# Kernel tuning notes

Measured on AMD Instinct MI355X. Metric: run time of the kernel, lower is better.

Reference implementation:

```python
import jax, jax.numpy as jnp
import numpy as np
import math

LEVELS = 10
T = 4096              # 2**log2_hashmap_size, log2=12
F = 2                 # n_features_per_level
NMIN, NMAX = 16, 320
HIDDEN = 512
OMEGA = 30.0
COOR_DIM = LEVELS * F + 2   # 22: hash feats + raw coords
_b = math.exp((math.log(NMAX) - math.log(NMIN)) / (LEVELS - 1))
RES = [int(math.floor(NMIN * _b ** l)) for l in range(LEVELS)]
PRIME_Y = np.uint32(2654435761)
MASK = np.uint32(T - 1)


def _hash2(xi, yi):
    # instant-NGP style spatial hash for 2D, uint32 wraparound arithmetic
    return (xi ^ (yi * PRIME_Y)) & MASK


def hash_encode(coords, table):
    # coords: [N,2] in [0,1); table: [LEVELS, T, F]
    feats = []
    for l in range(LEVELS):
        x = coords * RES[l]               # [N,2] continuous grid coords
        x0 = jnp.floor(x)
        w = x - x0                        # bilinear weights in [0,1)
        xi = x0.astype(jnp.uint32)
        x0i, y0i = xi[:, 0], xi[:, 1]
        x1i, y1i = x0i + np.uint32(1), y0i + np.uint32(1)
        tab = table[l]
        f00 = tab[_hash2(x0i, y0i)]       # [N,F] gathers
        f10 = tab[_hash2(x1i, y0i)]
        f01 = tab[_hash2(x0i, y1i)]
        f11 = tab[_hash2(x1i, y1i)]
        wx = w[:, 0:1]
        wy = w[:, 1:2]
        fx0 = f00 + (f10 - f00) * wx
        fx1 = f01 + (f11 - f01) * wx
        feats.append(fx0 + (fx1 - fx0) * wy)
    return jnp.concatenate(feats + [coords], axis=-1)  # [N, COOR_DIM]


def sine(x, w, b):
    # SineLayer.forward: sin(linear(x)); omega_0 is baked into first-layer init
    return jnp.sin(x @ w.T + b)


def _sine_init(key, out_f, in_f, is_first):
    kw, kb = jax.random.split(key)
    if is_first:
        lim = OMEGA / in_f
    else:
        lim = math.sqrt(6.0 / in_f) / OMEGA
    w = jax.random.uniform(kw, (out_f, in_f), jnp.float32, -lim, lim)
    blim = 1.0 / math.sqrt(in_f)
    b = jax.random.uniform(kb, (out_f,), jnp.float32, -blim, blim)
    return w, b


def setup_inputs() -> dict:
    key = jax.random.key(0)
    ks = jax.random.split(key, 8)
    N = 262144
    coords = jax.random.uniform(ks[0], (N, 2), jnp.float32)
    table = jax.random.uniform(ks[1], (LEVELS, T, F), jnp.float32, -1e-4, 1e-4)
    w1, b1 = _sine_init(ks[2], HIDDEN, COOR_DIM, True)
    w2, b2 = _sine_init(ks[3], HIDDEN, HIDDEN, False)
    ws1, bs1 = _sine_init(ks[4], HIDDEN, COOR_DIM + HIDDEN, False)
    ws2, bs2 = _sine_init(ks[5], HIDDEN, HIDDEN, False)
    wo, bo = _sine_init(ks[6], 2, HIDDEN, False)
    return {"coords": coords, "table": table,
            "w1": w1, "b1": b1, "w2": w2, "b2": b2,
            "ws1": ws1, "bs1": bs1, "ws2": ws2, "bs2": bs2,
            "wo": wo, "bo": bo}


def reference(coords, table, w1, b1, w2, b2, ws1, bs1, ws2, bs2, wo, bo):
    h0 = hash_encode(coords, table)            # [N,22]
    h1 = sine(sine(h0, w1, b1), w2, b2)        # first block (n_flayer=2)
    h2 = jnp.concatenate([h1, h0], axis=-1)    # skip connection [N,534]
    h2 = sine(sine(h2, ws1, bs1), ws2, bs2)    # second block (n_slayer=2)
    return sine(h2, wo, bo)                    # [N,2]
```

## Files before the change

kernel.cpp:

```cpp
#include <hip/hip_runtime.h>
#include <hip/hip_bf16.h>
#include <math.h>

#define MBLK    64
#define CHUNK   4096
#define H0_OFF  65536
#define LDSB    (H0_OFF + CHUNK)
#define INV2PI  0.15915494309189535f

#define OFF_W1  0
#define OFF_W2  16384
#define OFF_WS1 (16384+262144)
#define OFF_WS2 (278528+278528)
#define OFF_WO  (557056+262144)
#define NPACK   (819200+8192)

typedef __attribute__((ext_vector_type(8))) short bf16x8;
typedef __attribute__((ext_vector_type(4))) float f32x4;

struct ResArr { int r[10]; };

__device__ __forceinline__ unsigned short f2bf(float f) {
    unsigned u = __float_as_uint(f);
    u += 0x7FFFu + ((u >> 16) & 1u);
    return (unsigned short)(u >> 16);
}
__device__ __forceinline__ float bf2f(unsigned short h) {
    return __uint_as_float(((unsigned)h) << 16);
}
__device__ __forceinline__ float hwsin(float x) {
    float r;
    asm("v_sin_f32 %0, %1" : "=v"(r) : "v"(x));
    return r;
}
__device__ __forceinline__ unsigned pack_bf16_rne(float a, float b) {
    unsigned ua = __float_as_uint(a);
    unsigned ub = __float_as_uint(b);
    ua += 0x7FFFu + ((ua >> 16) & 1u);
    ub += 0x7FFFu + ((ub >> 16) & 1u);
    return __builtin_amdgcn_perm(ub, ua, 0x07060302u);
}

__global__ void pack_weights(const float* __restrict__ w1, const float* __restrict__ w2,
                             const float* __restrict__ ws1, const float* __restrict__ ws2,
                             const float* __restrict__ wo, unsigned short* __restrict__ out)
{
    int i = blockIdx.x * 256 + threadIdx.x;
    if (i >= NPACK) return;
    float v;
    if (i < OFF_WO) {
        int il, KC, K_src, K_valid;
        const float* src;
        if (i < OFF_W2)       { il = i;           KC = 1;  K_src = 22;  K_valid = 22;  src = w1;  }
        else if (i < OFF_WS1) { il = i - OFF_W2;  KC = 16; K_src = 512; K_valid = 512; src = w2;  }
        else if (i < OFF_WS2) { il = i - OFF_WS1; KC = 17; K_src = 534; K_valid = 534; src = ws1; }
        else                  { il = i - OFF_WS2; KC = 16; K_src = 512; K_valid = 512; src = ws2; }
        int blk  = il >> 9, idx = il & 511;
        int lane = idx >> 3, j = idx & 7;
        int nf   = blk & 3;
        int rest = blk >> 2;
        int c    = rest % KC;
        int nb   = rest / KC;
        int n = nb * 64 + nf * 16 + (lane & 15);
        int k = c * 32 + (lane >> 4) * 8 + j;
        v = (k < K_valid) ? src[n * K_src + k] : 0.f;
    } else {
        int j = i - OFF_WO;
        int h = j >> 12, ks = (j >> 9) & 7, lane = (j >> 3) & 63, jj = j & 7;
        int n = lane & 15;
        int k = h * 256 + ks * 32 + (lane >> 4) * 8 + jj;
        v = (n < 2) ? wo[n * 512 + k] : 0.f;
    }
    out[i] = f2bf(v * INV2PI);
}

template<int KSTEPS, bool TAIL, bool PREBAR>
__device__ __forceinline__ void mlp_layer(char* sm, const unsigned short* __restrict__ Wl,
                                          const float* __restrict__ bias,
                                          int wid, int lane)
{
    constexpr int NC = KSTEPS + (TAIL ? 1 : 0);
    const int n0 = wid * 64;
    const int lm = lane & 15;
    const int lk = lane >> 4;
    const int sw = (lm & 7) << 4;
    const int rbase = (lm*64 + lk*16) ^ sw;

    const unsigned short* up = Wl + (unsigned)(__builtin_amdgcn_readfirstlane(wid) * NC) * 2048;
    const int lo8 = lane << 3;

    f32x4 acc[4][4];
    #pragma unroll
    for (int i = 0; i < 4; ++i)
        #pragma unroll
        for (int j = 0; j < 4; ++j) { f32x4 z = {0.f,0.f,0.f,0.f}; acc[i][j] = z; }

    const char* ab = sm + rbase;
    #pragma unroll 1
    for (int ks = 0; ks < KSTEPS; ++ks) {
        bf16x8 w[4], a[4];
        #pragma unroll
        for (int nf = 0; nf < 4; ++nf)
            w[nf] = *(const bf16x8*)(up + nf*512 + lo8);
        #pragma unroll
        for (int mf = 0; mf < 4; ++mf)
            a[mf] = *(const bf16x8*)(ab + mf*1024);
        #pragma unroll
        for (int mf = 0; mf < 4; ++mf)
            #pragma unroll
            for (int nf = 0; nf < 4; ++nf)
                acc[mf][nf] = __builtin_amdgcn_mfma_f32_16x16x32_bf16(w[nf], a[mf], acc[mf][nf], 0, 0, 0);
        up += 2048;
        ab += CHUNK;
    }
    if (TAIL) {
        bf16x8 w[4], a[4];
        #pragma unroll
        for (int nf = 0; nf < 4; ++nf)
            w[nf] = *(const bf16x8*)(up + nf*512 + lo8);
        #pragma unroll
        for (int mf = 0; mf < 4; ++mf)
            a[mf] = *(const bf16x8*)(sm + H0_OFF + rbase + mf*1024);
        #pragma unroll
        for (int mf = 0; mf < 4; ++mf)
            #pragma unroll
            for (int nf = 0; nf < 4; ++nf)
                acc[mf][nf] = __builtin_amdgcn_mfma_f32_16x16x32_bf16(w[nf], a[mf], acc[mf][nf], 0, 0, 0);
    }

    if (PREBAR) __syncthreads();

    int R[4], C[4];
    #pragma unroll
    for (int mf = 0; mf < 4; ++mf)
        R[mf] = ((mf*16 + lm) * 64) ^ (sw & 64);
    #pragma unroll
    for (int nf = 0; nf < 4; ++nf)
        C[nf] = (((nf & 1)*32 + lk*8) ^ (sw & 48)) + (wid*2 + (nf >> 1)) * CHUNK;

    #pragma unroll
    for (int nf = 0; nf < 4; ++nf) {
        const float4 bv = *(const float4*)(bias + n0 + nf*16 + lk*4);
        #pragma unroll
        for (int mf = 0; mf < 4; ++mf) {
            float s0 = hwsin(fmaf(bv.x, INV2PI, acc[mf][nf][0]));
            float s1 = hwsin(fmaf(bv.y, INV2PI, acc[mf][nf][1]));
            float s2 = hwsin(fmaf(bv.z, INV2PI, acc[mf][nf][2]));
            float s3 = hwsin(fmaf(bv.w, INV2PI, acc[mf][nf][3]));
            uint2 pk;
            pk.x = pack_bf16_rne(s0, s1);
            pk.y = pack_bf16_rne(s2, s3);
            *(uint2*)(sm + (R[mf] + C[nf])) = pk;
        }
    }
    __syncthreads();
}

__global__ __launch_bounds__(512) __attribute__((amdgpu_waves_per_eu(4))) void siren_fused(
    const float* __restrict__ coords, const float* __restrict__ table,
    const float* __restrict__ b1, const float* __restrict__ b2,
    const float* __restrict__ bs1, const float* __restrict__ bs2,
    const float* __restrict__ bo,
    const unsigned short* __restrict__ Wp,
    float* __restrict__ outp,
    ResArr res)
{
    extern __shared__ char sm[];
    const int tid = threadIdx.x;
    const int pbase = blockIdx.x * MBLK;

    {
        int p  = tid & 63;
        int lg = tid >> 6;
        float2 cc = ((const float2*)coords)[pbase + p];
        #pragma unroll
        for (int li = 0; li < 2; ++li) {
            int l = lg + 8 * li;
            if (l < 10) {
                float R  = (float)res.r[l];
                float fx = cc.x * R, fy = cc.y * R;
                float x0 = floorf(fx), y0 = floorf(fy);
                float wx = fx - x0,  wy = fy - y0;
                unsigned xi = (unsigned)x0, yi = (unsigned)y0;
                unsigned yp  = yi * 2654435761u;
                unsigned yp1 = (yi + 1u) * 2654435761u;
                unsigned h00 = (xi        ^ yp ) & 4095u;
                unsigned h10 = ((xi + 1u) ^ yp ) & 4095u;
                unsigned h01 = (xi        ^ yp1) & 4095u;
                unsigned h11 = ((xi + 1u) ^ yp1) & 4095u;
                const float2* tl = (const float2*)(table + l * 8192);
                float2 f00 = tl[h00], f10 = tl[h10], f01 = tl[h01], f11 = tl[h11];
                float a0 = f00.x + (f10.x - f00.x) * wx;
                float a1 = f01.x + (f11.x - f01.x) * wx;
                float g0 = a0 + (a1 - a0) * wy;
                float c0 = f00.y + (f10.y - f00.y) * wx;
                float c1 = f01.y + (f11.y - f01.y) * wx;
                float g1 = c0 + (c1 - c0) * wy;
                unsigned pk = (unsigned)f2bf(g0) | ((unsigned)f2bf(g1) << 16);
                *(unsigned*)(sm + H0_OFF + (((p << 6) + 4*l) ^ ((p & 7) << 4))) = pk;
            }
        }
        if (lg == 2) {
            unsigned pk = (unsigned)f2bf(cc.x) | ((unsigned)f2bf(cc.y) << 16);
            *(unsigned*)(sm + H0_OFF + (((p << 6) + 40) ^ ((p & 7) << 4))) = pk;
        }
        if (lg == 3) {
            #pragma unroll
            for (int bb = 44; bb < 64; bb += 4)
                *(unsigned*)(sm + H0_OFF + (((p << 6) + bb) ^ ((p & 7) << 4))) = 0u;
        }
    }
    __syncthreads();

    const int wid  = tid >> 6;
    const int lane = tid & 63;

    mlp_layer<0,  true,  false>(sm, Wp + OFF_W1,  b1,  wid, lane);
    mlp_layer<16, false, true >(sm, Wp + OFF_W2,  b2,  wid, lane);
    mlp_layer<16, true,  true >(sm, Wp + OFF_WS1, bs1, wid, lane);
    mlp_layer<16, false, true >(sm, Wp + OFF_WS2, bs2, wid, lane);

    {
        const int lm = lane & 15;
        const int lk = lane >> 4;
        const int r0 = (wid & 3) * 16;
        const int h  = __builtin_amdgcn_readfirstlane(wid) >> 2;
        const int rbase = (((r0 + lm)*64 + lk*16) ^ ((lm & 7) << 4)) + h*8*CHUNK;
        const unsigned short* uo = Wp + OFF_WO + h*4096;
        const int lo8 = lane << 3;

        f32x4 acc = {0.f, 0.f, 0.f, 0.f};
        #pragma unroll
        for (int ks = 0; ks < 8; ++ks) {
            bf16x8 w = *(const bf16x8*)(uo + ks*512 + lo8);
            bf16x8 a = *(const bf16x8*)(sm + rbase + ks*CHUNK);
            acc = __builtin_amdgcn_mfma_f32_16x16x32_bf16(w, a, acc, 0, 0, 0);
        }
        __syncthreads();
        if (lk == 0) {
            float2 part; part.x = acc[0]; part.y = acc[1];
            *(float2*)(sm + H0_OFF + (h*64 + r0 + lm)*8) = part;
        }
    }
    __syncthreads();
    if (tid < 64) {
        float2 p0 = *(const float2*)(sm + H0_OFF + tid*8);
        float2 p1 = *(const float2*)(sm + H0_OFF + 512 + tid*8);
        float2 o;
        o.x = hwsin(fmaf(bo[0], INV2PI, p0.x + p1.x));
        o.y = hwsin(fmaf(bo[1], INV2PI, p0.y + p1.y));
        ((float2*)outp)[pbase + tid] = o;
    }
}

extern "C" void kernel_launch(void* const* d_in, const int* in_sizes, int n_in,
                              void* d_out, int out_size, void* d_ws, size_t ws_size,
                              hipStream_t stream)
{
    const float* coords = (const float*)d_in[0];
    const float* table  = (const float*)d_in[1];
    const float* w1  = (const float*)d_in[2];
    const float* b1  = (const float*)d_in[3];
    const float* w2  = (const float*)d_in[4];
    const float* b2  = (const float*)d_in[5];
    const float* ws1 = (const float*)d_in[6];
    const float* bs1 = (const float*)d_in[7];
    const float* ws2 = (const float*)d_in[8];
    const float* bs2 = (const float*)d_in[9];
    const float* wo  = (const float*)d_in[10];
    const float* bo  = (const float*)d_in[11];

    unsigned short* Wp = (unsigned short*)d_ws;
    float* outp = (float*)d_out;

    ResArr res;
    double bb = exp((log(320.0) - log(16.0)) / 9.0);
    for (int l = 0; l < 10; ++l) res.r[l] = (int)floor(16.0 * pow(bb, (double)l));

    (void)hipFuncSetAttribute((const void*)siren_fused,
                              hipFuncAttributeMaxDynamicSharedMemorySize, LDSB);

    int N = in_sizes[0] / 2;

    pack_weights<<<(NPACK + 255) / 256, 256, 0, stream>>>(w1, w2, ws1, ws2, wo, Wp);
    siren_fused<<<N / MBLK, 512, LDSB, stream>>>(coords, table, b1, b2, bs1, bs2, bo,
                                                 Wp, outp, res);
}
```

Measured before the change: 373.0 us.

## Switch MLP layers to 32x32x16 MFMA tiles with repacked weights

Replaces the 16x16x32 bf16 MFMA tiling (4x4 fragments per wave) with 32x32x16 MFMA (2x2 fragments), repacks the weight layout to match, and changes the LDS activation read/write addressing and swizzle to suit. The sine epilogue is now computed before the pre-barrier, and the packed results are stored to LDS after it, so transcendental work can overlap other waves' MMA. The larger MFMA instruction issues fewer instructions per FLOP, at the cost of holding all packed results in registers across the barrier, which raises register pressure.

```diff
diff --git a/kernel.cpp b/kernel.cpp
--- a/kernel.cpp
+++ b/kernel.cpp
@@ -15,8 +15,9 @@
 #define OFF_WO  (557056+262144)
 #define NPACK   (819200+8192)
 
-typedef __attribute__((ext_vector_type(8))) short bf16x8;
-typedef __attribute__((ext_vector_type(4))) float f32x4;
+typedef __attribute__((ext_vector_type(8)))  short bf16x8;
+typedef __attribute__((ext_vector_type(4)))  float f32x4;
+typedef __attribute__((ext_vector_type(16))) float f32x16;
 
 struct ResArr { int r[10]; };
 
@@ -49,20 +50,20 @@
     if (i >= NPACK) return;
     float v;
     if (i < OFF_WO) {
-        int il, KC, K_src, K_valid;
+        int il, NC2, K_src, K_valid;
         const float* src;
-        if (i < OFF_W2)       { il = i;           KC = 1;  K_src = 22;  K_valid = 22;  src = w1;  }
-        else if (i < OFF_WS1) { il = i - OFF_W2;  KC = 16; K_src = 512; K_valid = 512; src = w2;  }
-        else if (i < OFF_WS2) { il = i - OFF_WS1; KC = 17; K_src = 534; K_valid = 534; src = ws1; }
-        else                  { il = i - OFF_WS2; KC = 16; K_src = 512; K_valid = 512; src = ws2; }
+        if (i < OFF_W2)       { il = i;           NC2 = 2;  K_src = 22;  K_valid = 22;  src = w1;  }
+        else if (i < OFF_WS1) { il = i - OFF_W2;  NC2 = 32; K_src = 512; K_valid = 512; src = w2;  }
+        else if (i < OFF_WS2) { il = i - OFF_WS1; NC2 = 34; K_src = 534; K_valid = 534; src = ws1; }
+        else                  { il = i - OFF_WS2; NC2 = 32; K_src = 512; K_valid = 512; src = ws2; }
         int blk  = il >> 9, idx = il & 511;
         int lane = idx >> 3, j = idx & 7;
-        int nf   = blk & 3;
-        int rest = blk >> 2;
-        int c    = rest % KC;
-        int nb   = rest / KC;
-        int n = nb * 64 + nf * 16 + (lane & 15);
-        int k = c * 32 + (lane >> 4) * 8 + j;
+        int nr   = blk & 1;
+        int rest = blk >> 1;
+        int c    = rest % NC2;
+        int nb   = rest / NC2;
+        int n = nb * 64 + nr * 32 + (lane & 31);
+        int k = c * 16 + (lane >> 5) * 8 + j;
         v = (k < K_valid) ? src[n * K_src + k] : 0.f;
     } else {
         int j = i - OFF_WO;
@@ -74,85 +75,96 @@
     out[i] = f2bf(v * INV2PI);
 }
 
-template<int KSTEPS, bool TAIL, bool PREBAR>
+template<int CHUNKS, bool TAIL, bool PREBAR>
 __device__ __forceinline__ void mlp_layer(char* sm, const unsigned short* __restrict__ Wl,
                                           const float* __restrict__ bias,
                                           int wid, int lane)
 {
-    constexpr int NC = KSTEPS + (TAIL ? 1 : 0);
-    const int n0 = wid * 64;
-    const int lm = lane & 15;
-    const int lk = lane >> 4;
-    const int sw = (lm & 7) << 4;
-    const int rbase = (lm*64 + lk*16) ^ sw;
-
-    const unsigned short* up = Wl + (unsigned)(__builtin_amdgcn_readfirstlane(wid) * NC) * 2048;
-    const int lo8 = lane << 3;
-
-    f32x4 acc[4][4];
+    constexpr int NC2 = 2*CHUNKS + (TAIL ? 2 : 0);
+    const int n0  = wid * 64;
+    const int l31 = lane & 31;
+    const int hi  = lane >> 5;
+    const int sw  = (l31 & 7) << 4;
+    const int rb  = (l31*64 + hi*16) ^ sw;
+
+    const unsigned short* up = Wl + (unsigned)(wid * NC2) * 1024 + (lane << 3);
+
+    f32x16 acc[2][2];
     #pragma unroll
-    for (int i = 0; i < 4; ++i)
-        #pragma unroll
-        for (int j = 0; j < 4; ++j) { f32x4 z = {0.f,0.f,0.f,0.f}; acc[i][j] = z; }
-
-    const char* ab = sm + rbase;
+    for (int mr = 0; mr < 2; ++mr)
+        #pragma unroll
+        for (int nr = 0; nr < 2; ++nr)
+            #pragma unroll
+            for (int e = 0; e < 16; ++e) acc[mr][nr][e] = 0.f;
+
+    int ao = rb;
     #pragma unroll 1
-    for (int ks = 0; ks < KSTEPS; ++ks) {
-        bf16x8 w[4], a[4];
-        #pragma unroll
-        for (int nf = 0; nf < 4; ++nf)
-            w[nf] = *(const bf16x8*)(up + nf*512 + lo8);
-        #pragma unroll
-        for (int mf = 0; mf < 4; ++mf)
-            a[mf] = *(const bf16x8*)(ab + mf*1024);
-        #pragma unroll
-        for (int mf = 0; mf < 4; ++mf)
+    for (int c = 0; c < CHUNKS; ++c) {
+        bf16x8 w0a = *(const bf16x8*)(up + 0);
+        bf16x8 w0b = *(const bf16x8*)(up + 512);
+        bf16x8 w1a = *(const bf16x8*)(up + 1024);
+        bf16x8 w1b = *(const bf16x8*)(up + 1536);
+        bf16x8 a00 = *(const bf16x8*)(sm + ao);
+        bf16x8 a01 = *(const bf16x8*)(sm + ao + 2048);
+        bf16x8 a10 = *(const bf16x8*)(sm + (ao ^ 32));
+        bf16x8 a11 = *(const bf16x8*)(sm + (ao ^ 32) + 2048);
+        acc[0][0] = __builtin_amdgcn_mfma_f32_32x32x16_bf16(w0a, a00, acc[0][0], 0, 0, 0);
+        acc[1][0] = __builtin_amdgcn_mfma_f32_32x32x16_bf16(w0a, a01, acc[1][0], 0, 0, 0);
+        acc[0][1] = __builtin_amdgcn_mfma_f32_32x32x16_bf16(w0b, a00, acc[0][1], 0, 0, 0);
+        acc[1][1] = __builtin_amdgcn_mfma_f32_32x32x16_bf16(w0b, a01, acc[1][1], 0, 0, 0);
+        acc[0][0] = __builtin_amdgcn_mfma_f32_32x32x16_bf16(w1a, a10, acc[0][0], 0, 0, 0);
+        acc[1][0] = __builtin_amdgcn_mfma_f32_32x32x16_bf16(w1a, a11, acc[1][0], 0, 0, 0);
+        acc[0][1] = __builtin_amdgcn_mfma_f32_32x32x16_bf16(w1b, a10, acc[0][1], 0, 0, 0);
+        acc[1][1] = __builtin_amdgcn_mfma_f32_32x32x16_bf16(w1b, a11, acc[1][1], 0, 0, 0);
+        up += 2048;
+        ao += CHUNK;
+    }
+    if (TAIL) {
+        const int ho = H0_OFF + rb;
+        bf16x8 w0a = *(const bf16x8*)(up + 0);
+        bf16x8 w0b = *(const bf16x8*)(up + 512);
+        bf16x8 w1a = *(const bf16x8*)(up + 1024);
+        bf16x8 w1b = *(const bf16x8*)(up + 1536);
+        bf16x8 a00 = *(const bf16x8*)(sm + ho);
+        bf16x8 a01 = *(const bf16x8*)(sm + ho + 2048);
+        bf16x8 a10 = *(const bf16x8*)(sm + (ho ^ 32));
+        bf16x8 a11 = *(const bf16x8*)(sm + (ho ^ 32) + 2048);
+        acc[0][0] = __builtin_amdgcn_mfma_f32_32x32x16_bf16(w0a, a00, acc[0][0], 0, 0, 0);
+        acc[1][0] = __builtin_amdgcn_mfma_f32_32x32x16_bf16(w0a, a01, acc[1][0], 0, 0, 0);
+        acc[0][1] = __builtin_amdgcn_mfma_f32_32x32x16_bf16(w0b, a00, acc[0][1], 0, 0, 0);
+        acc[1][1] = __builtin_amdgcn_mfma_f32_32x32x16_bf16(w0b, a01, acc[1][1], 0, 0, 0);
+        acc[0][0] = __builtin_amdgcn_mfma_f32_32x32x16_bf16(w1a, a10, acc[0][0], 0, 0, 0);
+        acc[1][0] = __builtin_amdgcn_mfma_f32_32x32x16_bf16(w1a, a11, acc[1][0], 0, 0, 0);
+        acc[0][1] = __builtin_amdgcn_mfma_f32_32x32x16_bf16(w1b, a10, acc[0][1], 0, 0, 0);
+        acc[1][1] = __builtin_amdgcn_mfma_f32_32x32x16_bf16(w1b, a11, acc[1][1], 0, 0, 0);
+    }
+
+    uint2 pk[2][2][4];
+    #pragma unroll
+    for (int mr = 0; mr < 2; ++mr)
+        #pragma unroll
+        for (int nr = 0; nr < 2; ++nr)
             #pragma unroll
-            for (int nf = 0; nf < 4; ++nf)
-                acc[mf][nf] = __builtin_amdgcn_mfma_f32_16x16x32_bf16(w[nf], a[mf], acc[mf][nf], 0, 0, 0);
-        up += 2048;
-        ab += CHUNK;
-    }
-    if (TAIL) {
-        bf16x8 w[4], a[4];
-        #pragma unroll
-        for (int nf = 0; nf < 4; ++nf)
-            w[nf] = *(const bf16x8*)(up + nf*512 + lo8);
-        #pragma unroll
-        for (int mf = 0; mf < 4; ++mf)
-            a[mf] = *(const bf16x8*)(sm + H0_OFF + rbase + mf*1024);
-        #pragma unroll
-        for (int mf = 0; mf < 4; ++mf)
+            for (int q = 0; q < 4; ++q) {
+                const float4 bv = *(const float4*)(bias + n0 + nr*32 + q*8 + hi*4);
+                float s0 = hwsin(fmaf(bv.x, INV2PI, acc[mr][nr][q*4+0]));
+                float s1 = hwsin(fmaf(bv.y, INV2PI, acc[mr][nr][q*4+1]));
+                float s2 = hwsin(fmaf(bv.z, INV2PI, acc[mr][nr][q*4+2]));
+                float s3 = hwsin(fmaf(bv.w, INV2PI, acc[mr][nr][q*4+3]));
+                pk[mr][nr][q].x = pack_bf16_rne(s0, s1);
+                pk[mr][nr][q].y = pack_bf16_rne(s2, s3);
+            }
+
+    if (PREBAR) __syncthreads();
+
+    const int wb = (l31*64 + 8*hi) ^ sw;
+    #pragma unroll
+    for (int mr = 0; mr < 2; ++mr)
+        #pragma unroll
+        for (int nr = 0; nr < 2; ++nr)
             #pragma unroll
-            for (int nf = 0; nf < 4; ++nf)
-                acc[mf][nf] = __builtin_amdgcn_mfma_f32_16x16x32_bf16(w[nf], a[mf], acc[mf][nf], 0, 0, 0);
-    }
-
-    if (PREBAR) __syncthreads();
-
-    int R[4], C[4];
-    #pragma unroll
-    for (int mf = 0; mf < 4; ++mf)
-        R[mf] = ((mf*16 + lm) * 64) ^ (sw & 64);
-    #pragma unroll
-    for (int nf = 0; nf < 4; ++nf)
-        C[nf] = (((nf & 1)*32 + lk*8) ^ (sw & 48)) + (wid*2 + (nf >> 1)) * CHUNK;
-
-    #pragma unroll
-    for (int nf = 0; nf < 4; ++nf) {
-        const float4 bv = *(const float4*)(bias + n0 + nf*16 + lk*4);
-        #pragma unroll
-        for (int mf = 0; mf < 4; ++mf) {
-            float s0 = hwsin(fmaf(bv.x, INV2PI, acc[mf][nf][0]));
-            float s1 = hwsin(fmaf(bv.y, INV2PI, acc[mf][nf][1]));
-            float s2 = hwsin(fmaf(bv.z, INV2PI, acc[mf][nf][2]));
-            float s3 = hwsin(fmaf(bv.w, INV2PI, acc[mf][nf][3]));
-            uint2 pk;
-            pk.x = pack_bf16_rne(s0, s1);
-            pk.y = pack_bf16_rne(s2, s3);
-            *(uint2*)(sm + (R[mf] + C[nf])) = pk;
-        }
-    }
+            for (int q = 0; q < 4; ++q)
+                *(uint2*)(sm + ((wb ^ (q << 4)) + (wid*2 + nr)*CHUNK + mr*2048)) = pk[mr][nr][q];
     __syncthreads();
 }
 
```

Result: slower. 411.9 us (+10.4%).
